# Kernel optimization log

Measured on AMD Instinct MI355X. Metric: run time of the kernel, lower is better.

The kernel has to match this reference:

```python
import math
import jax, jax.numpy as jnp
import numpy as np

B, S, D, H = 2, 2048, 1024, 16
HD = D // H
I = 3752  # round(1024 * 11/3 / 8) * 8, per GluMLP default
EPS = 1e-6


def _alibi_bias(nheads, n):
    # AlibiPostionEmbedding: slopes (power-of-2 formula) * -1, times |i-j|
    start = 2.0 ** (-(2.0 ** (-(math.log2(nheads) - 3))))
    slopes = np.array([start * start ** i for i in range(nheads)], dtype=np.float64) * -1.0
    pos = np.arange(n)
    rel = np.abs(pos[None, :] - pos[:, None])  # [n, n]
    return jnp.asarray(slopes[:, None, None] * rel[None, :, :], dtype=jnp.float32)


def rmsnorm(h, w):
    h32 = h.astype(jnp.float32)
    var = jnp.mean(h32 * h32, axis=-1, keepdims=True)
    return (w * (h32 * jax.lax.rsqrt(var + EPS))).astype(h.dtype)


def setup_inputs() -> dict:
    key = jax.random.key(0)
    ks = jax.random.split(key, 16)
    sd = 1.0 / math.sqrt(D)
    si = 1.0 / math.sqrt(I)
    rn = lambda k, shape, s: jax.random.normal(k, shape, jnp.float32) * s
    return {
        "x": rn(ks[0], (B, S, D), 1.0),
        "wq": rn(ks[1], (D, D), sd), "bq": rn(ks[2], (D,), 0.02),
        "wk": rn(ks[3], (D, D), sd), "bk": rn(ks[4], (D,), 0.02),
        "wv": rn(ks[5], (D, D), sd), "bv": rn(ks[6], (D,), 0.02),
        "wo": rn(ks[7], (D, D), sd), "bo": rn(ks[8], (D,), 0.02),
        "w_gate": rn(ks[9], (D, I), sd),
        "w_up": rn(ks[10], (D, I), sd),
        "w_down": rn(ks[11], (I, D), si),
        "ln1_w": jnp.ones((D,), jnp.float32),
        "ln2_w": jnp.ones((D,), jnp.float32),
        "attn_bias": _alibi_bias(H, S),                       # [H, S, S]
        "tgt_mask": jnp.triu(jnp.ones((S, S), bool), 1),      # causal, True = masked
        "key_padding_mask": jnp.zeros((B, S), bool),          # True = padded
    }


def reference(x, wq, bq, wk, bk, wv, bv, wo, bo, w_gate, w_up, w_down,
              ln1_w, ln2_w, attn_bias, tgt_mask, key_padding_mask):
    # ---- TransformerEncoderLayer.forward (eval mode: dropout = identity) ----
    residual = x
    h = rmsnorm(x, ln1_w)
    # MultiheadAttention with ALiBi bias + fused bool masks
    q = (h @ wq + bq).reshape(B, S, H, HD)
    k = (h @ wk + bk).reshape(B, S, H, HD)
    v = (h @ wv + bv).reshape(B, S, H, HD)
    scores = jnp.einsum("bqhd,bkhd->bhqk", q, k) * (HD ** -0.5)  # [B,H,S,S]
    scores = scores + attn_bias[None]
    mask = tgt_mask[None, :, :] | key_padding_mask[:, None, :]   # [B,S,S]
    scores = jnp.where(mask[:, None, :, :], -jnp.inf, scores)
    probs = jax.nn.softmax(scores, axis=-1)
    attn = jnp.einsum("bhqk,bkhd->bqhd", probs, v).reshape(B, S, D)
    attn = attn @ wo + bo
    residual = attn + residual
    # GluMLP (SwiGLU)
    h2 = rmsnorm(residual, ln2_w)
    mlp = (jax.nn.silu(h2 @ w_gate) * (h2 @ w_up)) @ w_down
    return mlp + residual
```

## Files before the change

### kernel.cpp

```cpp
#include <hip/hip_runtime.h>
#include <hip/hip_bf16.h>
#include <cmath>

typedef __bf16 bf16_t;
typedef __bf16 bf16x8 __attribute__((ext_vector_type(8)));
typedef short  s16x8  __attribute__((ext_vector_type(8)));
typedef float  f32x4  __attribute__((ext_vector_type(4)));

static constexpr int Bn  = 2;
static constexpr int Sn  = 2048;
static constexpr int Dn  = 1024;
static constexpr int Hn  = 16;
static constexpr int In  = 3752;
static constexpr int Mn  = Bn * Sn;

__device__ __forceinline__ void cp16(const bf16_t* g, bf16_t* l) {
  __builtin_amdgcn_global_load_lds(
      (const __attribute__((address_space(1))) unsigned int*)g,
      (__attribute__((address_space(3))) unsigned int*)l, 16, 0, 0);
}

__global__ __launch_bounds__(256) void k_transpose(const float* __restrict__ in,
                                                   bf16_t* __restrict__ out,
                                                   int R, int C) {
  __shared__ float tile[32][33];
  const int c0 = blockIdx.x * 32, r0 = blockIdx.y * 32;
  const int tx = threadIdx.x & 31, ty = threadIdx.x >> 5;
#pragma unroll
  for (int e = 0; e < 4; ++e) {
    int r = r0 + ty + e * 8, c = c0 + tx;
    if (r < R && c < C) tile[ty + e * 8][tx] = in[(size_t)r * C + c];
  }
  __syncthreads();
#pragma unroll
  for (int e = 0; e < 4; ++e) {
    int c = c0 + ty + e * 8, r = r0 + tx;
    if (r < R && c < C) out[(size_t)c * R + r] = (bf16_t)tile[tx][ty + e * 8];
  }
}

__global__ __launch_bounds__(256) void k_rmsnorm(const float* __restrict__ in,
                                                 const float* __restrict__ w,
                                                 bf16_t* __restrict__ out) {
  const int row = blockIdx.x;
  const int tid = threadIdx.x;
  const float* ip = in + (size_t)row * Dn;
  float v[4];
  float ss = 0.f;
#pragma unroll
  for (int e = 0; e < 4; ++e) {
    v[e] = ip[tid + e * 256];
    ss += v[e] * v[e];
  }
  for (int off = 32; off > 0; off >>= 1) ss += __shfl_down(ss, off);
  __shared__ float red[4];
  if ((tid & 63) == 0) red[tid >> 6] = ss;
  __syncthreads();
  float tot = red[0] + red[1] + red[2] + red[3];
  float sc = rsqrtf(tot * (1.0f / Dn) + 1e-6f);
  bf16_t* op = out + (size_t)row * Dn;
#pragma unroll
  for (int e = 0; e < 4; ++e) {
    int idx = tid + e * 256;
    op[idx] = (bf16_t)(w[idx] * v[e] * sc);
  }
}

__global__ __launch_bounds__(256) void k_gemm(
    const bf16_t* __restrict__ A, const bf16_t* __restrict__ Bt,
    const float* __restrict__ bias, const float* __restrict__ resid,
    float* __restrict__ outf, int N, int K, int lda, int ldb, int mode) {
  __shared__ bf16_t As[128 * 64];
  __shared__ bf16_t Bs[128 * 64];
  const int m0 = blockIdx.x * 128, n0 = blockIdx.y * 128;
  const int tid = threadIdx.x;
  const int lane = tid & 63, wid = tid >> 6;
  const int wr = (wid >> 1) * 64, wc = (wid & 1) * 64;
  const int l15 = lane & 15, quad = lane >> 4;
  const int sw = l15 & 7;
  const int srow_lo = lane >> 3;
  const int pchunk  = lane & 7;

  f32x4 acc[4][4];
  const f32x4 z4 = {0.f, 0.f, 0.f, 0.f};
#pragma unroll
  for (int i = 0; i < 4; ++i)
#pragma unroll
    for (int j = 0; j < 4; ++j) acc[i][j] = z4;

  for (int k0 = 0; k0 < K; k0 += 64) {
#pragma unroll
    for (int c = 0; c < 4; ++c) {
      const int r = (wid * 4 + c) * 8 + srow_lo;
      const int gc = pchunk ^ (r & 7);
      cp16(A  + (size_t)(m0 + r) * lda + k0 + gc * 8, As + (wid * 4 + c) * 512);
      cp16(Bt + (size_t)(n0 + r) * ldb + k0 + gc * 8, Bs + (wid * 4 + c) * 512);
    }
    __syncthreads();
#pragma unroll
    for (int kh = 0; kh < 2; ++kh) {
      bf16x8 af[4], bfr[4];
      const int ph = ((kh * 4 + quad) ^ sw) * 8;
#pragma unroll
      for (int i = 0; i < 4; ++i)
        af[i] = *(const bf16x8*)(As + (wr + i * 16 + l15) * 64 + ph);
#pragma unroll
      for (int j = 0; j < 4; ++j)
        bfr[j] = *(const bf16x8*)(Bs + (wc + j * 16 + l15) * 64 + ph);
#pragma unroll
      for (int i = 0; i < 4; ++i)
#pragma unroll
        for (int j = 0; j < 4; ++j)
          acc[i][j] = __builtin_amdgcn_mfma_f32_16x16x32_bf16(af[i], bfr[j], acc[i][j], 0, 0, 0);
    }
    __syncthreads();
  }

#pragma unroll
  for (int i = 0; i < 4; ++i)
#pragma unroll
    for (int j = 0; j < 4; ++j) {
      const int col = n0 + wc + j * 16 + l15;
      const float bval = bias ? bias[col] : 0.f;
#pragma unroll
      for (int r = 0; r < 4; ++r) {
        const int row = m0 + wr + i * 16 + quad * 4 + r;
        const size_t idx = (size_t)row * N + col;
        const float v = acc[i][j][r] + bval;
        if (mode == 1) outf[idx] = v + (resid ? resid[idx] : 0.f);
        else           outf[idx] += v;
      }
    }
}

__global__ __launch_bounds__(256) void k_gemm_qkv(
    const bf16_t* __restrict__ A, const bf16_t* __restrict__ Bt,
    const float* __restrict__ bq, const float* __restrict__ bk,
    const float* __restrict__ bv,
    bf16_t* __restrict__ qk, bf16_t* __restrict__ vt) {
  __shared__ bf16_t As[128 * 64];
  __shared__ bf16_t Bs[128 * 64];
  const int m0 = blockIdx.x * 128, n0 = blockIdx.y * 128;
  const int tid = threadIdx.x;
  const int lane = tid & 63, wid = tid >> 6;
  const int wr = (wid >> 1) * 64, wc = (wid & 1) * 64;
  const int l15 = lane & 15, quad = lane >> 4;
  const int sw = l15 & 7;
  const int srow_lo = lane >> 3, pchunk = lane & 7;

  f32x4 acc[4][4];
  const f32x4 z4 = {0.f, 0.f, 0.f, 0.f};
#pragma unroll
  for (int i = 0; i < 4; ++i)
#pragma unroll
    for (int j = 0; j < 4; ++j) acc[i][j] = z4;

  for (int k0 = 0; k0 < Dn; k0 += 64) {
#pragma unroll
    for (int c = 0; c < 4; ++c) {
      const int r = (wid * 4 + c) * 8 + srow_lo;
      const int gc = pchunk ^ (r & 7);
      cp16(A  + (size_t)(m0 + r) * Dn + k0 + gc * 8, As + (wid * 4 + c) * 512);
      cp16(Bt + (size_t)(n0 + r) * Dn + k0 + gc * 8, Bs + (wid * 4 + c) * 512);
    }
    __syncthreads();
#pragma unroll
    for (int kh = 0; kh < 2; ++kh) {
      bf16x8 af[4], bfr[4];
      const int ph = ((kh * 4 + quad) ^ sw) * 8;
#pragma unroll
      for (int i = 0; i < 4; ++i)
        af[i] = *(const bf16x8*)(As + (wr + i * 16 + l15) * 64 + ph);
#pragma unroll
      for (int j = 0; j < 4; ++j)
        bfr[j] = *(const bf16x8*)(Bs + (wc + j * 16 + l15) * 64 + ph);
#pragma unroll
      for (int i = 0; i < 4; ++i)
#pragma unroll
        for (int j = 0; j < 4; ++j)
          acc[i][j] = __builtin_amdgcn_mfma_f32_16x16x32_bf16(af[i], bfr[j], acc[i][j], 0, 0, 0);
    }
    __syncthreads();
  }

#pragma unroll
  for (int i = 0; i < 4; ++i)
#pragma unroll
    for (int j = 0; j < 4; ++j) {
      const int col = n0 + wc + j * 16 + l15;
      const int sel = col >> 10;
      const float bval = (sel == 0) ? bq[col] : (sel == 1) ? bk[col - 1024] : bv[col - 2048];
#pragma unroll
      for (int r = 0; r < 4; ++r) {
        const int row = m0 + wr + i * 16 + quad * 4 + r;
        const float v = acc[i][j][r] + bval;
        if (sel < 2) {
          qk[(size_t)row * 2048 + col] = (bf16_t)v;
        } else {
          const int dd = col & 63, hh = (col >> 6) & 15;
          const int bb = row >> 11, ss = row & 2047;
          vt[(size_t)((bb * 16 + hh) * 64 + dd) * 2048 + ss] = (bf16_t)v;
        }
      }
    }
}

__global__ __launch_bounds__(256) void k_gemm_gateup(
    const bf16_t* __restrict__ A, const bf16_t* __restrict__ Bg,
    const bf16_t* __restrict__ Bu, bf16_t* __restrict__ out, int N) {
  __shared__ bf16_t As[128 * 64];
  __shared__ bf16_t Gs[128 * 64];
  __shared__ bf16_t Us[128 * 64];
  const int m0 = blockIdx.x * 128, n0 = blockIdx.y * 128;
  const int tid = threadIdx.x;
  const int lane = tid & 63, wid = tid >> 6;
  const int wr = (wid >> 1) * 64, wc = (wid & 1) * 64;
  const int l15 = lane & 15, quad = lane >> 4;
  const int sw = l15 & 7;
  const int srow_lo = lane >> 3, pchunk = lane & 7;

  f32x4 accg[4][4], accu[4][4];
  const f32x4 z4 = {0.f, 0.f, 0.f, 0.f};
#pragma unroll
  for (int i = 0; i < 4; ++i)
#pragma unroll
    for (int j = 0; j < 4; ++j) { accg[i][j] = z4; accu[i][j] = z4; }

  for (int k0 = 0; k0 < Dn; k0 += 64) {
#pragma unroll
    for (int c = 0; c < 4; ++c) {
      const int r = (wid * 4 + c) * 8 + srow_lo;
      const int gc = pchunk ^ (r & 7);
      const int nb = min(n0 + r, N - 1);
      cp16(A  + (size_t)(m0 + r) * Dn + k0 + gc * 8, As + (wid * 4 + c) * 512);
      cp16(Bg + (size_t)nb * Dn + k0 + gc * 8, Gs + (wid * 4 + c) * 512);
      cp16(Bu + (size_t)nb * Dn + k0 + gc * 8, Us + (wid * 4 + c) * 512);
    }
    __syncthreads();
#pragma unroll
    for (int kh = 0; kh < 2; ++kh) {
      bf16x8 af[4], gf[4], uf[4];
      const int ph = ((kh * 4 + quad) ^ sw) * 8;
#pragma unroll
      for (int i = 0; i < 4; ++i)
        af[i] = *(const bf16x8*)(As + (wr + i * 16 + l15) * 64 + ph);
#pragma unroll
      for (int j = 0; j < 4; ++j) {
        gf[j] = *(const bf16x8*)(Gs + (wc + j * 16 + l15) * 64 + ph);
        uf[j] = *(const bf16x8*)(Us + (wc + j * 16 + l15) * 64 + ph);
      }
#pragma unroll
      for (int i = 0; i < 4; ++i)
#pragma unroll
        for (int j = 0; j < 4; ++j) {
          accg[i][j] = __builtin_amdgcn_mfma_f32_16x16x32_bf16(af[i], gf[j], accg[i][j], 0, 0, 0);
          accu[i][j] = __builtin_amdgcn_mfma_f32_16x16x32_bf16(af[i], uf[j], accu[i][j], 0, 0, 0);
        }
    }
    __syncthreads();
  }

#pragma unroll
  for (int i = 0; i < 4; ++i)
#pragma unroll
    for (int j = 0; j < 4; ++j) {
      const int col = n0 + wc + j * 16 + l15;
#pragma unroll
      for (int r = 0; r < 4; ++r) {
        const int row = m0 + wr + i * 16 + quad * 4 + r;
        const float g = accg[i][j][r];
        const float u = accu[i][j][r];
        const float sl = g / (1.f + expf(-g));
        out[(size_t)row * 1024 + col] = (col < N) ? (bf16_t)(sl * u) : (bf16_t)0.f;
      }
    }
}

__global__ __launch_bounds__(256) void k_attn(
    const bf16_t* __restrict__ qk, const bf16_t* __restrict__ vt,
    bf16_t* __restrict__ Ob) {
  const int qt = (int)gridDim.x - 1 - (int)blockIdx.x;
  const int h  = blockIdx.y;
  const int b  = blockIdx.z;
  constexpr int LDK = 72;
  constexpr int LDP = 76;
  __shared__ bf16_t Ks[64 * LDK];
  __shared__ bf16_t Vt[64 * LDK];
  __shared__ bf16_t Ps[4][16 * LDP];

  const int tid  = threadIdx.x;
  const int lane = tid & 63, w = tid >> 6;
  const int l15  = lane & 15, quad = lane >> 4;

  constexpr float L2E = 1.4426950408889634f;
  const float slopeL = -exp2f(-0.5f * (float)(h + 1)) * L2E;

  const int qrow_frag = qt * 64 + w * 16 + l15;
  const size_t qbase = (size_t)(b * Sn + qrow_frag) * 2048 + h * 64;
  bf16x8 aq0 = *(const bf16x8*)(qk + qbase + quad * 8);
  bf16x8 aq1 = *(const bf16x8*)(qk + qbase + 32 + quad * 8);
#pragma unroll
  for (int e = 0; e < 8; ++e) {
    aq0[e] = (bf16_t)((float)aq0[e] * 0.125f);
    aq1[e] = (bf16_t)((float)aq1[e] * 0.125f);
  }

  const int qrow0 = qt * 64 + w * 16 + quad * 4;
  float Atr[4][4];
#pragma unroll
  for (int t = 0; t < 4; ++t)
#pragma unroll
    for (int rr = 0; rr < 4; ++rr)
      Atr[t][rr] = slopeL * (float)(qrow0 + rr - (t * 16 + l15));
  const float kstepL = slopeL * 64.f;

  f32x4 o[4], lacc;
  const f32x4 z4 = {0.f, 0.f, 0.f, 0.f};
#pragma unroll
  for (int dt = 0; dt < 4; ++dt) o[dt] = z4;
  lacc = z4;
  bf16x8 ones;
#pragma unroll
  for (int e = 0; e < 8; ++e) ones[e] = (bf16_t)1.0f;

  const int r = tid >> 2, c0e = (tid & 3) * 16;
  const size_t kbase = (size_t)(b * Sn + r) * 2048 + 1024 + h * 64 + c0e;
  const size_t vbase = (size_t)((b * 16 + h) * 64 + r) * 2048 + c0e;

  s16x8 kr0 = *(const s16x8*)(qk + kbase);
  s16x8 kr1 = *(const s16x8*)(qk + kbase + 8);
  s16x8 vr0 = *(const s16x8*)(vt + vbase);
  s16x8 vr1 = *(const s16x8*)(vt + vbase + 8);

  const int nkt = qt + 1;
  for (int kt = 0; kt < nkt; ++kt) {
    __syncthreads();
    *(s16x8*)(Ks + r * LDK + c0e)     = kr0;
    *(s16x8*)(Ks + r * LDK + c0e + 8) = kr1;
    *(s16x8*)(Vt + r * LDK + c0e)     = vr0;
    *(s16x8*)(Vt + r * LDK + c0e + 8) = vr1;
    __syncthreads();
    if (kt + 1 < nkt) {
      const size_t gkn = kbase + (size_t)(kt + 1) * (64 * 2048);
      kr0 = *(const s16x8*)(qk + gkn);
      kr1 = *(const s16x8*)(qk + gkn + 8);
      const size_t gvn = vbase + (size_t)(kt + 1) * 64;
      vr0 = *(const s16x8*)(vt + gvn);
      vr1 = *(const s16x8*)(vt + gvn + 8);
    }

    f32x4 s[4];
#pragma unroll
    for (int t = 0; t < 4; ++t) s[t] = z4;
#pragma unroll
    for (int t = 0; t < 4; ++t) {
      bf16x8 bk0 = *(const bf16x8*)(Ks + (t * 16 + l15) * LDK + quad * 8);
      bf16x8 bk1 = *(const bf16x8*)(Ks + (t * 16 + l15) * LDK + 32 + quad * 8);
      s[t] = __builtin_amdgcn_mfma_f32_16x16x32_bf16(aq0, bk0, s[t], 0, 0, 0);
      s[t] = __builtin_amdgcn_mfma_f32_16x16x32_bf16(aq1, bk1, s[t], 0, 0, 0);
    }

    const float ko = kstepL * (float)kt;
    const bool diag = (kt == qt);
#pragma unroll
    for (int t = 0; t < 4; ++t) {
      const int j = kt * 64 + t * 16 + l15;
#pragma unroll
      for (int rr = 0; rr < 4; ++rr) {
        float v2 = fmaf(s[t][rr], L2E, Atr[t][rr] - ko);
        if (diag && j > qrow0 + rr) v2 = -3.0e38f;
        Ps[w][(quad * 4 + rr) * LDP + t * 16 + l15] = (bf16_t)exp2f(v2);
      }
    }

#pragma unroll
    for (int kh = 0; kh < 2; ++kh) {
      bf16x8 pa = *(const bf16x8*)(Ps[w] + l15 * LDP + kh * 32 + quad * 8);
      lacc = __builtin_amdgcn_mfma_f32_16x16x32_bf16(pa, ones, lacc, 0, 0, 0);
#pragma unroll
      for (int dt = 0; dt < 4; ++dt) {
        bf16x8 bv = *(const bf16x8*)(Vt + (dt * 16 + l15) * LDK + kh * 32 + quad * 8);
        o[dt] = __builtin_amdgcn_mfma_f32_16x16x32_bf16(pa, bv, o[dt], 0, 0, 0);
      }
    }
  }

#pragma unroll
  for (int rr = 0; rr < 4; ++rr) {
    const float inv = 1.f / lacc[rr];
    bf16_t* op = Ob + ((size_t)(b * Sn + qrow0 + rr) * Hn + h) * 64;
#pragma unroll
    for (int dt = 0; dt < 4; ++dt)
      op[dt * 16 + l15] = (bf16_t)(o[dt][rr] * inv);
  }
}

extern "C" void kernel_launch(void* const* d_in, const int* in_sizes, int n_in,
                              void* d_out, int out_size, void* d_ws, size_t ws_size,
                              hipStream_t stream) {
  (void)in_sizes; (void)n_in; (void)out_size; (void)ws_size;
  const float* x   = (const float*)d_in[0];
  const float* wq  = (const float*)d_in[1];
  const float* bq  = (const float*)d_in[2];
  const float* wk_ = (const float*)d_in[3];
  const float* bk  = (const float*)d_in[4];
  const float* wv  = (const float*)d_in[5];
  const float* bv  = (const float*)d_in[6];
  const float* wo  = (const float*)d_in[7];
  const float* bo  = (const float*)d_in[8];
  const float* wg  = (const float*)d_in[9];
  const float* wu  = (const float*)d_in[10];
  const float* wd  = (const float*)d_in[11];
  const float* ln1 = (const float*)d_in[12];
  const float* ln2 = (const float*)d_in[13];

  char* base = (char*)d_ws;
  const size_t SLOT = 8u * 1024 * 1024;
  bf16_t* h1     = (bf16_t*)(base);
  bf16_t* wqkvT  = (bf16_t*)(base + SLOT);
  bf16_t* qkb    = (bf16_t*)(base + 2 * SLOT);
  float*  res1   = (float*) (base + 2 * SLOT);
  bf16_t* vt     = (bf16_t*)(base + 4 * SLOT);
  bf16_t* chunk0 = (bf16_t*)(base + 5 * SLOT);
  bf16_t* wgT    = h1;
  bf16_t* woT    = wqkvT;
  bf16_t* wuT    = wqkvT;
  bf16_t* wdT    = vt;
  bf16_t* attnb  = (bf16_t*)d_out;
  bf16_t* h2     = (bf16_t*)d_out;

  const dim3 blk(256);
  const dim3 gT(Dn / 32, Dn / 32);
  const dim3 gD(Mn / 128, Dn / 128);

  k_rmsnorm<<<dim3(Mn), blk, 0, stream>>>(x, ln1, h1);

  k_transpose<<<gT, blk, 0, stream>>>(wq,  wqkvT, Dn, Dn);
  k_transpose<<<gT, blk, 0, stream>>>(wk_, wqkvT + (size_t)Dn * Dn, Dn, Dn);
  k_transpose<<<gT, blk, 0, stream>>>(wv,  wqkvT + 2 * (size_t)Dn * Dn, Dn, Dn);

  k_gemm_qkv<<<dim3(Mn / 128, 3072 / 128), blk, 0, stream>>>(h1, wqkvT, bq, bk, bv, qkb, vt);

  k_attn<<<dim3(Sn / 64, Hn, Bn), blk, 0, stream>>>(qkb, vt, attnb);

  k_transpose<<<gT, blk, 0, stream>>>(wo, woT, Dn, Dn);
  k_gemm<<<gD, blk, 0, stream>>>(attnb, woT, bo, x, res1, Dn, Dn, Dn, Dn, 1);

  k_rmsnorm<<<dim3(Mn), blk, 0, stream>>>(res1, ln2, h2);

  k_transpose<<<dim3((In + 31) / 32, Dn / 32), blk, 0, stream>>>(wg, wgT, Dn, In);
  k_transpose<<<dim3((In + 31) / 32, Dn / 32), blk, 0, stream>>>(wu, wuT, Dn, In);
  k_transpose<<<dim3(Dn / 32, (In + 31) / 32), blk, 0, stream>>>(wd, wdT, In, Dn);
  const int c0s[4]   = {0, 1024, 2048, 3072};
  const int cns[4]   = {1024, 1024, 1024, In - 3072};
  const int kpads[4] = {1024, 1024, 1024, 768};
  for (int c = 0; c < 4; ++c) {
    const int c0 = c0s[c], cn = cns[c], kp = kpads[c];
    k_gemm_gateup<<<dim3(Mn / 128, kp / 128), blk, 0, stream>>>(
        h2, wgT + (size_t)c0 * Dn, wuT + (size_t)c0 * Dn, chunk0, cn);
    if (c < 3) {
      k_gemm<<<gD, blk, 0, stream>>>(chunk0, wdT + c0, nullptr, nullptr,
                                     res1, Dn, kp, 1024, In, 4);
    } else {
      k_gemm<<<gD, blk, 0, stream>>>(chunk0, wdT + c0, nullptr, res1,
                                     (float*)d_out, Dn, kp, 1024, In, 1);
    }
  }
}
```

Measured before the change: 837.9 us.

## Unchunk SwiGLU MLP into single gate-up and down GEMMs with 64-row tiles

The four-chunk MLP loop is replaced by one gate/up GEMM covering the whole intermediate dimension, padded to 3840, into a dedicated buffer. One down-projection GEMM with K=3840 then adds the residual directly. The output-projection and down-projection GEMMs switch to a 64x128 tile kernel, which doubles the block count on the GPU. This is meant to cut launches, avoid repeated fp32 read-modify-write of the accumulator, and improve CU utilisation. The cost is a larger intermediate buffer and less reuse per block from the smaller tiles.

```diff
diff --git a/kernel.cpp b/kernel.cpp
--- a/kernel.cpp
+++ b/kernel.cpp
@@ -13,6 +13,7 @@
 static constexpr int Hn  = 16;
 static constexpr int In  = 3752;
 static constexpr int Mn  = Bn * Sn;
+static constexpr int Ipad = 3840;
 
 __device__ __forceinline__ void cp16(const bf16_t* g, bf16_t* l) {
   __builtin_amdgcn_global_load_lds(
@@ -66,51 +67,55 @@
   }
 }
 
-__global__ __launch_bounds__(256) void k_gemm(
+__global__ __launch_bounds__(256) void k_gemm64(
     const bf16_t* __restrict__ A, const bf16_t* __restrict__ Bt,
     const float* __restrict__ bias, const float* __restrict__ resid,
-    float* __restrict__ outf, int N, int K, int lda, int ldb, int mode) {
-  __shared__ bf16_t As[128 * 64];
+    float* __restrict__ outf, int N, int K, int lda, int ldb) {
+  __shared__ bf16_t As[64 * 64];
   __shared__ bf16_t Bs[128 * 64];
-  const int m0 = blockIdx.x * 128, n0 = blockIdx.y * 128;
+  const int m0 = blockIdx.x * 64, n0 = blockIdx.y * 128;
   const int tid = threadIdx.x;
   const int lane = tid & 63, wid = tid >> 6;
-  const int wr = (wid >> 1) * 64, wc = (wid & 1) * 64;
+  const int wc = wid * 32;
   const int l15 = lane & 15, quad = lane >> 4;
   const int sw = l15 & 7;
-  const int srow_lo = lane >> 3;
-  const int pchunk  = lane & 7;
-
-  f32x4 acc[4][4];
+  const int srow_lo = lane >> 3, pchunk = lane & 7;
+
+  f32x4 acc[4][2];
   const f32x4 z4 = {0.f, 0.f, 0.f, 0.f};
 #pragma unroll
   for (int i = 0; i < 4; ++i)
 #pragma unroll
-    for (int j = 0; j < 4; ++j) acc[i][j] = z4;
+    for (int j = 0; j < 2; ++j) acc[i][j] = z4;
 
   for (int k0 = 0; k0 < K; k0 += 64) {
+#pragma unroll
+    for (int c = 0; c < 2; ++c) {
+      const int r = (wid * 2 + c) * 8 + srow_lo;
+      const int gc = pchunk ^ (r & 7);
+      cp16(A + (size_t)(m0 + r) * lda + k0 + gc * 8, As + (wid * 2 + c) * 512);
+    }
 #pragma unroll
     for (int c = 0; c < 4; ++c) {
       const int r = (wid * 4 + c) * 8 + srow_lo;
       const int gc = pchunk ^ (r & 7);
-      cp16(A  + (size_t)(m0 + r) * lda + k0 + gc * 8, As + (wid * 4 + c) * 512);
       cp16(Bt + (size_t)(n0 + r) * ldb + k0 + gc * 8, Bs + (wid * 4 + c) * 512);
     }
     __syncthreads();
 #pragma unroll
     for (int kh = 0; kh < 2; ++kh) {
-      bf16x8 af[4], bfr[4];
       const int ph = ((kh * 4 + quad) ^ sw) * 8;
-#pragma unroll
-      for (int i = 0; i < 4; ++i)
-        af[i] = *(const bf16x8*)(As + (wr + i * 16 + l15) * 64 + ph);
-#pragma unroll
-      for (int j = 0; j < 4; ++j)
+      bf16x8 af[4], bfr[2];
+#pragma unroll
+      for (int i = 0; i < 4; ++i)
+        af[i] = *(const bf16x8*)(As + (i * 16 + l15) * 64 + ph);
+#pragma unroll
+      for (int j = 0; j < 2; ++j)
         bfr[j] = *(const bf16x8*)(Bs + (wc + j * 16 + l15) * 64 + ph);
 #pragma unroll
       for (int i = 0; i < 4; ++i)
 #pragma unroll
-        for (int j = 0; j < 4; ++j)
+        for (int j = 0; j < 2; ++j)
           acc[i][j] = __builtin_amdgcn_mfma_f32_16x16x32_bf16(af[i], bfr[j], acc[i][j], 0, 0, 0);
     }
     __syncthreads();
@@ -119,16 +124,14 @@
 #pragma unroll
   for (int i = 0; i < 4; ++i)
 #pragma unroll
-    for (int j = 0; j < 4; ++j) {
+    for (int j = 0; j < 2; ++j) {
       const int col = n0 + wc + j * 16 + l15;
       const float bval = bias ? bias[col] : 0.f;
 #pragma unroll
       for (int r = 0; r < 4; ++r) {
-        const int row = m0 + wr + i * 16 + quad * 4 + r;
+        const int row = m0 + i * 16 + quad * 4 + r;
         const size_t idx = (size_t)row * N + col;
-        const float v = acc[i][j][r] + bval;
-        if (mode == 1) outf[idx] = v + (resid ? resid[idx] : 0.f);
-        else           outf[idx] += v;
+        outf[idx] = acc[i][j][r] + bval + (resid ? resid[idx] : 0.f);
       }
     }
 }
@@ -207,7 +210,7 @@
 
 __global__ __launch_bounds__(256) void k_gemm_gateup(
     const bf16_t* __restrict__ A, const bf16_t* __restrict__ Bg,
-    const bf16_t* __restrict__ Bu, bf16_t* __restrict__ out, int N) {
+    const bf16_t* __restrict__ Bu, bf16_t* __restrict__ out, int N, int ldo) {
   __shared__ bf16_t As[128 * 64];
   __shared__ bf16_t Gs[128 * 64];
   __shared__ bf16_t Us[128 * 64];
@@ -271,7 +274,7 @@
         const float g = accg[i][j][r];
         const float u = accu[i][j][r];
         const float sl = g / (1.f + expf(-g));
-        out[(size_t)row * 1024 + col] = (col < N) ? (bf16_t)(sl * u) : (bf16_t)0.f;
+        out[(size_t)row * ldo + col] = (col < N) ? (bf16_t)(sl * u) : (bf16_t)0.f;
       }
     }
 }
@@ -415,13 +418,13 @@
   const float* ln2 = (const float*)d_in[13];
 
   char* base = (char*)d_ws;
-  const size_t SLOT = 8u * 1024 * 1024;
+  const size_t MiB = 1024 * 1024;
   bf16_t* h1     = (bf16_t*)(base);
-  bf16_t* wqkvT  = (bf16_t*)(base + SLOT);
-  bf16_t* qkb    = (bf16_t*)(base + 2 * SLOT);
-  float*  res1   = (float*) (base + 2 * SLOT);
-  bf16_t* vt     = (bf16_t*)(base + 4 * SLOT);
-  bf16_t* chunk0 = (bf16_t*)(base + 5 * SLOT);
+  bf16_t* wqkvT  = (bf16_t*)(base + 8 * MiB);
+  bf16_t* qkb    = (bf16_t*)(base + 16 * MiB);
+  float*  res1   = (float*) (base + 16 * MiB);
+  bf16_t* vt     = (bf16_t*)(base + 32 * MiB);
+  bf16_t* mlp    = (bf16_t*)(base + 40 * MiB);
   bf16_t* wgT    = h1;
   bf16_t* woT    = wqkvT;
   bf16_t* wuT    = wqkvT;
@@ -431,7 +434,6 @@
 
   const dim3 blk(256);
   const dim3 gT(Dn / 32, Dn / 32);
-  const dim3 gD(Mn / 128, Dn / 128);
 
   k_rmsnorm<<<dim3(Mn), blk, 0, stream>>>(x, ln1, h1);
 
@@ -444,26 +446,18 @@
   k_attn<<<dim3(Sn / 64, Hn, Bn), blk, 0, stream>>>(qkb, vt, attnb);
 
   k_transpose<<<gT, blk, 0, stream>>>(wo, woT, Dn, Dn);
-  k_gemm<<<gD, blk, 0, stream>>>(attnb, woT, bo, x, res1, Dn, Dn, Dn, Dn, 1);
+  k_gemm64<<<dim3(Mn / 64, Dn / 128), blk, 0, stream>>>(
+      attnb, woT, bo, x, res1, Dn, Dn, Dn, Dn);
 
   k_rmsnorm<<<dim3(Mn), blk, 0, stream>>>(res1, ln2, h2);
 
   k_transpose<<<dim3((In + 31) / 32, Dn / 32), blk, 0, stream>>>(wg, wgT, Dn, In);
   k_transpose<<<dim3((In + 31) / 32, Dn / 32), blk, 0, stream>>>(wu, wuT, Dn, In);
   k_transpose<<<dim3(Dn / 32, (In + 31) / 32), blk, 0, stream>>>(wd, wdT, In, Dn);
-  const int c0s[4]   = {0, 1024, 2048, 3072};
-  const int cns[4]   = {1024, 1024, 1024, In - 3072};
-  const int kpads[4] = {1024, 1024, 1024, 768};
-  for (int c = 0; c < 4; ++c) {
-    const int c0 = c0s[c], cn = cns[c], kp = kpads[c];
-    k_gemm_gateup<<<dim3(Mn / 128, kp / 128), blk, 0, stream>>>(
-        h2, wgT + (size_t)c0 * Dn, wuT + (size_t)c0 * Dn, chunk0, cn);
-    if (c < 3) {
-      k_gemm<<<gD, blk, 0, stream>>>(chunk0, wdT + c0, nullptr, nullptr,
-                                     res1, Dn, kp, 1024, In, 4);
-    } else {
-      k_gemm<<<gD, blk, 0, stream>>>(chunk0, wdT + c0, nullptr, res1,
-                                     (float*)d_out, Dn, kp, 1024, In, 1);
-    }
-  }
-}
+
+  k_gemm_gateup<<<dim3(Mn / 128, Ipad / 128), blk, 0, stream>>>(
+      h2, wgT, wuT, mlp, In, Ipad);
+
+  k_gemm64<<<dim3(Mn / 64, Dn / 128), blk, 0, stream>>>(
+      mlp, wdT, nullptr, res1, (float*)d_out, Dn, Ipad, Ipad, In);
+}
```

Measured after the change: 743.9 us. 1.13x faster.
